# Performance work log

Hardware: AMD Instinct MI355X
Metric: run time of the kernel (lower is better)

Reference implementation:

```python
import jax, jax.numpy as jnp
import numpy as np

N_HEADS = 12
MAX_POS = 2048
SEQ = MAX_POS - 2  # seq_len_without_special = 2046
HEAD_DIM = 64
BATCH = 8


def setup_inputs() -> dict:
    key = jax.random.key(0)
    k1, k2, k3 = jax.random.split(key, 3)
    v = jax.random.normal(k1, (BATCH, MAX_POS, N_HEADS, HEAD_DIM), jnp.float32)
    offset = jax.random.normal(k2, (1, N_HEADS), jnp.float32)
    # learned bias base, torch init: uniform(-0.1, 0.1), shape [1, H, SEQ] (symmetric)
    w = jax.random.uniform(k3, (1, N_HEADS, SEQ), jnp.float32, -0.1, 0.1)
    return {"v": v, "offset": offset, "w": w}


def _fft_bias(v, offset, w):
    # strip special tokens ([CLS]/[SEP])
    v_ = v[:, 1:-1, :, :]                      # [B, S, H, D]
    B, S, H, D = v_.shape
    # --- symmetric circulant base z of length 2S-1 ---
    w_ = w[..., :S]                            # [1, H, S]
    z = jnp.concatenate(
        [w_[..., -1:], jnp.flip(w_[..., 1:], axis=-1), w_[..., :-1]], axis=-1
    )                                          # [1, H, 2S-1]
    z = z - offset[..., None]                  # broadcast offset per head
    z = jnp.exp(z)                             # feature_map == 'exp'
    z_fft = jnp.fft.rfft(z)                    # [1, H, S] complex (len 2S-1 odd -> m=S)

    pad = S - 1                                # symmetric: pad_size = seq_len - 1
    v_p = jnp.transpose(v_, (0, 3, 2, 1))      # [B, D, H, S]
    v_p = jnp.pad(v_p, ((0, 0), (0, 0), (0, 0), (pad, 0)))  # left-pad to 2S-1
    v_fft = jnp.fft.rfft(v_p)                  # [B, D, H, S]
    # torch.irfft(x, 1) with default signal_sizes infers even length 2*(m-1)=2S-2
    pbv = jnp.fft.irfft(v_fft * z_fft)[..., :S]  # [B, D, H, S]
    pbv = jnp.pad(pbv, ((0, 0), (0, 0), (0, 0), (1, 1)))     # restore special slots
    pbv = jnp.transpose(pbv, (0, 3, 2, 1))     # [B, S+2, H, D]

    o = jnp.pad(jnp.ones((S,), v.dtype), (pad, 0))           # [2S-1]
    o_fft = jnp.fft.rfft(o)                    # [S]
    z_pb = jnp.fft.irfft(z_fft * o_fft)[..., :S]             # [1, H, S]
    z_pb = jnp.pad(z_pb, ((0, 0), (0, 0), (1, 1)))           # [1, H, S+2]
    z_pb = jnp.swapaxes(z_pb, -2, -1)          # [1, S+2, H]
    return pbv, z_pb


def reference(v, offset, w):
    return _fft_bias(v, offset, w)
```

## Files before the change

### kernel.cpp

```cpp
#include <hip/hip_runtime.h>
#include <hip/hip_bf16.h>

#define BATCH 8
#define MAXPOS 2048
#define SEQ 2046
#define NH 12
#define HD 64
#define NCSLOT 254
#define TSTEPS 64
#define PLANE (NH * HD)

typedef __attribute__((ext_vector_type(4))) float floatx4;
typedef __attribute__((ext_vector_type(8))) short shortx8;

#define ATILE_BYTES (NH * NCSLOT * 512 * 2)

#define GLOAD_LDS16(src, dst)                                                  \
    __builtin_amdgcn_global_load_lds(                                          \
        (const __attribute__((address_space(1))) void*)(src),                  \
        (__attribute__((address_space(3))) void*)(dst), 16, 0, 0)

#define NB_V2  (BATCH * TSTEPS)
#define NB_ZPB NH
#define NB_A   (NCSLOT * NH)

__global__ __launch_bounds__(256)
void prep_all(const float* __restrict__ v, const float* __restrict__ w,
              const float* __restrict__ off, ushort* __restrict__ atile,
              ushort* __restrict__ vbf, float* __restrict__ out) {
    __shared__ __align__(16) char smem[32 * 768 * 2];
    const int bi  = blockIdx.x;
    const int tid = threadIdx.x;

    if (bi < NB_V2) {
        ushort (*L)[768] = (ushort(*)[768])smem;
        const int b  = bi >> 6;
        const int tc = bi & 63;
        const int t0 = tc * 32;
        const float* vb = v + (size_t)(b * MAXPOS + 1 + t0) * PLANE;
#pragma unroll
        for (int i = 0; i < 24; ++i) {
            const int f = i * 256 + tid;
            const int r = f / 192;
            const int s = f - r * 192;
            float4 val = make_float4(0.f, 0.f, 0.f, 0.f);
            if (t0 + r < SEQ) val = *(const float4*)(vb + (size_t)f * 4);
            __hip_bfloat16 c0 = __float2bfloat16(val.x);
            __hip_bfloat16 c1 = __float2bfloat16(val.y);
            __hip_bfloat16 c2 = __float2bfloat16(val.z);
            __hip_bfloat16 c3 = __float2bfloat16(val.w);
            ushort4 pk;
            pk.x = *(ushort*)&c0; pk.y = *(ushort*)&c1;
            pk.z = *(ushort*)&c2; pk.w = *(ushort*)&c3;
            *(ushort4*)&L[r][(s * 4) ^ ((r >> 3) * 16)] = pk;
        }
        __syncthreads();
        const int wv   = tid >> 6;
        const int lane = tid & 63;
        const int q    = lane >> 4;
        const int dcol = lane & 15;
        const int cb   = wv * 16 + dcol;
#pragma unroll
        for (int h = 0; h < NH; ++h) {
            const int pc = (h * 64 + cb) ^ (q * 16);
            ushort pk[8];
#pragma unroll
            for (int j = 0; j < 8; ++j) pk[j] = L[q * 8 + j][pc];
            *(uint4*)(vbf + ((size_t)((b * NH + h) * TSTEPS + tc) * 4 + wv) * 512 + lane * 8) = *(uint4*)pk;
        }
    } else if (bi < NB_V2 + NB_ZPB) {
        float* Es   = (float*)smem;
        float* Ss   = (float*)smem + 2048;
        float* wsum = (float*)smem + 4096;
        const int h    = bi - NB_V2;
        const int wid  = tid >> 6;
        const int lane = tid & 63;
        const float offh = off[h];
        const float* wh  = w + h * SEQ;
        for (int i = tid; i < SEQ; i += 256) Es[i] = __expf(wh[i] - offh);
        __syncthreads();
        const int base = tid * 8;
        float loc[8];
        float s = 0.f;
#pragma unroll
        for (int j = 0; j < 8; ++j) {
            float e = (base + j < SEQ) ? Es[base + j] : 0.f;
            s += e; loc[j] = s;
        }
        float sc = s;
#pragma unroll
        for (int d = 1; d < 64; d <<= 1) {
            float t = __shfl_up(sc, d);
            if (lane >= d) sc += t;
        }
        if (lane == 63) wsum[wid] = sc;
        __syncthreads();
        float woff = 0.f;
        for (int k = 0; k < wid; ++k) woff += wsum[k];
        float prefix = woff + sc - s;
#pragma unroll
        for (int j = 0; j < 8; ++j)
            if (base + j < SEQ) Ss[base + j] = prefix + loc[j];
        __syncthreads();
        const float E0 = Es[0];
        const size_t zb = (size_t)BATCH * MAXPOS * PLANE;
        for (int i = tid; i < SEQ; i += 256)
            out[zb + (size_t)(i + 1) * NH + h] = Ss[i] + Ss[SEQ - 1 - i] - E0;
    } else if (bi < NB_V2 + NB_ZPB + NB_A) {
        const int idx   = bi - NB_V2 - NB_ZPB;
        const int cslot = idx % NCSLOT;
        const int h     = idx / NCSLOT;
        const float offh = off[h];
        const float* wh  = w + h * SEQ;
        const int ci   = cslot - 127;
        const int lane = tid >> 2;
        const int jp   = (tid & 3) * 2;
        const int q    = lane >> 4;
        const int m    = lane & 15;
        const int d0   = 16 * ci + q * 8 - m + jp;
        ushort pk[2];
#pragma unroll
        for (int e = 0; e < 2; ++e) {
            int k = d0 + e; k = (k < 0) ? -k : k;
            float val = (k < SEQ) ? __expf(wh[k] - offh) : 0.f;
            __hip_bfloat16 bv = __float2bfloat16(val);
            pk[e] = *(ushort*)&bv;
        }
        *(ushort2*)(atile + ((size_t)(h * NCSLOT + cslot) * 512 + lane * 8 + jp)) = *(ushort2*)pk;
    } else {
        const int i = (bi - NB_V2 - NB_ZPB - NB_A) * 256 + tid;
        if (i < 2 * BATCH * PLANE) {
            int side = i / (BATCH * PLANE);
            int r    = i % (BATCH * PLANE);
            int b    = r / PLANE;
            int j    = r % PLANE;
            int p    = side ? (MAXPOS - 1) : 0;
            out[((size_t)b * MAXPOS + p) * PLANE + j] = 0.f;
        }
        if (i < 2 * NH) {
            size_t zb = (size_t)BATCH * MAXPOS * PLANE;
            int p = (i < NH) ? 0 : (MAXPOS - 1);
            out[zb + (size_t)p * NH + (i % NH)] = 0.f;
        }
    }
}


#define WBAR                                                                   \
  do {                                                                         \
    if (wvu < 2) asm volatile("s_waitcnt vmcnt(2)\n\ts_barrier" ::: "memory"); \
    else         asm volatile("s_waitcnt vmcnt(1)\n\ts_barrier" ::: "memory"); \
  } while (0)
#define WBAR0 asm volatile("s_waitcnt vmcnt(0)\n\ts_barrier" ::: "memory")

#define STEP(T4, E, STG)                                                       \
  do {                                                                         \
    const int abE = ab + 2 * (E);                                              \
    shortx8 bf[4];                                                             \
    a2 = a0; a3 = a1;                                                          \
    a0 = *(const shortx8*)(&As[(abE) & 31][lane8]);                            \
    a1 = *(const shortx8*)(&As[(abE - 1) & 31][lane8]);                        \
    _Pragma("unroll")                                                          \
    for (int dt = 0; dt < 4; ++dt)                                             \
        bf[dt] = *(const shortx8*)(&Bs[T4][dt][lane8]);                        \
    if (STG) {                                                                 \
        if (wvu < 2)                                                           \
            GLOAD_LDS16(aSt + (E) * 1024, &As[(csw + 2 * (E)) & 31][0]);       \
        GLOAD_LDS16(bSt + (E) * 2048, &Bs[((T4) + 2) & 3][wvu][0]);            \
    }                                                                          \
    __builtin_amdgcn_s_setprio(1);                                             \
    _Pragma("unroll")                                                          \
    for (int dt = 0; dt < 4; ++dt)                                             \
        acc[2][dt] = __builtin_amdgcn_mfma_f32_16x16x32_bf16(a2, bf[dt], acc[2][dt], 0, 0, 0); \
    _Pragma("unroll")                                                          \
    for (int dt = 0; dt < 4; ++dt)                                             \
        acc[3][dt] = __builtin_amdgcn_mfma_f32_16x16x32_bf16(a3, bf[dt], acc[3][dt], 0, 0, 0); \
    _Pragma("unroll")                                                          \
    for (int dt = 0; dt < 4; ++dt)                                             \
        acc[0][dt] = __builtin_amdgcn_mfma_f32_16x16x32_bf16(a0, bf[dt], acc[0][dt], 0, 0, 0); \
    _Pragma("unroll")                                                          \
    for (int dt = 0; dt < 4; ++dt)                                             \
        acc[1][dt] = __builtin_amdgcn_mfma_f32_16x16x32_bf16(a1, bf[dt], acc[1][dt], 0, 0, 0); \
    __builtin_amdgcn_s_setprio(0);                                             \
  } while (0)

__global__ __launch_bounds__(256, 3)
void gemm_pbv(const ushort* __restrict__ atile, const ushort* __restrict__ vbf,
              float* __restrict__ out) {
    __shared__ short As[32][512];
    __shared__ short Bs[4][4][512];

    const int bid  = blockIdx.x;
    const int l    = (bid & 7) * 96 + (bid >> 3);
    const int g    = l >> 3;
    const int nt   = l & 7;
    const int h    = g >> 3;
    const int bb   = g & 7;
    const int tid  = threadIdx.x;
    const int wvu  = __builtin_amdgcn_readfirstlane(tid >> 6);
    const int lane = tid & 63;
    const int lane8 = lane * 8;
    const int nt16  = nt * 16;

    floatx4 acc[4][4];
#pragma unroll
    for (int s = 0; s < 4; ++s)
#pragma unroll
        for (int dt = 0; dt < 4; ++dt) acc[s][dt] = (floatx4){0.f, 0.f, 0.f, 0.f};

    const ushort* aBase  = atile + (size_t)h * NCSLOT * 512;
    const ushort* bPanel = vbf + (size_t)(bb * NH + h) * (TSTEPS * 4 * 512);

    {
        const int cbase = 112 - nt16;
        const int j0 = (wvu == 0) ? 0 : (wvu == 1) ? 5 : (wvu == 2) ? 10 : 14;
        const int j1 = (wvu == 0) ? 5 : (wvu == 1) ? 10 : (wvu == 2) ? 14 : 18;
        for (int j = j0; j < j1; ++j) {
            const int cs = cbase + j;
            GLOAD_LDS16(aBase + (size_t)cs * 512 + lane8, &As[cs & 31][0]);
        }
        GLOAD_LDS16(bPanel + (0 * 4 + wvu) * 512 + lane8, &Bs[0][wvu][0]);
        GLOAD_LDS16(bPanel + (1 * 4 + wvu) * 512 + lane8, &Bs[1][wvu][0]);
    }
    WBAR0;

    int ab  = 127 - nt16 - 4 * wvu;
    int csw = 131 - nt16 - wvu;
    const ushort* aSt = aBase + (size_t)(131 - nt16 - wvu) * 512 + lane8;
    const ushort* bSt = bPanel + (2 * 4 + wvu) * 512 + lane8;

    shortx8 a0, a1, a2, a3;
    a0 = *(const shortx8*)(&As[(ab - 2) & 31][lane8]);
    a1 = *(const shortx8*)(&As[(ab - 3) & 31][lane8]);

    for (int u = 0; u < 15; ++u) {
        STEP(0, 0, 1); WBAR;
        STEP(1, 1, 1); WBAR;
        STEP(2, 2, 1); WBAR;
        STEP(3, 3, 1); WBAR;
        ab += 8; csw += 8; aSt += 4 * 1024; bSt += 4 * 2048;
    }
    STEP(0, 0, 1); WBAR;
    STEP(1, 1, 1); WBAR;
    STEP(2, 2, 0); WBAR0;
    STEP(3, 3, 0);

    const int q    = lane >> 4;
    const int dcol = lane & 15;
    const int nB   = nt * 256 + wvu * 64;
#pragma unroll
    for (int s = 0; s < 4; ++s) {
        int nsb = nB + s * 16 + q * 4;
#pragma unroll
        for (int r = 0; r < 4; ++r) {
            int n = nsb + r;
            if (n < SEQ) {
                float* ob = out + ((size_t)(bb * MAXPOS + 1 + n) * NH + h) * HD + dcol;
#pragma unroll
                for (int dt = 0; dt < 4; ++dt) ob[dt * 16] = acc[s][dt][r];
            }
        }
    }
}

extern "C" void kernel_launch(void* const* d_in, const int* in_sizes, int n_in,
                              void* d_out, int out_size, void* d_ws, size_t ws_size,
                              hipStream_t stream) {
    const float* v   = (const float*)d_in[0];
    const float* off = (const float*)d_in[1];
    const float* w   = (const float*)d_in[2];
    float* out = (float*)d_out;

    ushort* atile = (ushort*)d_ws;
    ushort* vbf   = (ushort*)((char*)d_ws + ATILE_BYTES);

    prep_all<<<NB_V2 + NB_ZPB + NB_A + 48, 256, 0, stream>>>(v, w, off, atile, vbf, out);
    gemm_pbv<<<768, 256, 0, stream>>>(atile, vbf, out);
}
```

Measured before the change: 135.7 us.

## Split prep kernel and software-pipeline GEMM fragment loads across barrier

The fused prep kernel becomes two kernels, one for the bf16 repack of v and one for the bias tile, zpb and zero-fill work, so each launch has uniform block types and smaller LDS use. The GEMM main loop now uses three-deep B staging and double-buffered A/B register fragments. The next step's LDS reads are issued between the two halves of the MFMA work, after the vmcnt wait, with a single barrier at the end of each step, so LDS latency hides behind MFMAs. This adds an extra kernel launch and more register pressure at three blocks per CU.

After: 142.1 us. 4.7% more time.

```diff
diff --git a/kernel.cpp b/kernel.cpp
--- a/kernel.cpp
+++ b/kernel.cpp
@@ -25,54 +25,57 @@
 #define NB_A   (NCSLOT * NH)
 
 __global__ __launch_bounds__(256)
-void prep_all(const float* __restrict__ v, const float* __restrict__ w,
-              const float* __restrict__ off, ushort* __restrict__ atile,
-              ushort* __restrict__ vbf, float* __restrict__ out) {
-    __shared__ __align__(16) char smem[32 * 768 * 2];
+void prep_v(const float* __restrict__ v, ushort* __restrict__ vbf) {
+    __shared__ __align__(16) ushort L[32][768];
     const int bi  = blockIdx.x;
     const int tid = threadIdx.x;
-
-    if (bi < NB_V2) {
-        ushort (*L)[768] = (ushort(*)[768])smem;
-        const int b  = bi >> 6;
-        const int tc = bi & 63;
-        const int t0 = tc * 32;
-        const float* vb = v + (size_t)(b * MAXPOS + 1 + t0) * PLANE;
-#pragma unroll
-        for (int i = 0; i < 24; ++i) {
-            const int f = i * 256 + tid;
-            const int r = f / 192;
-            const int s = f - r * 192;
-            float4 val = make_float4(0.f, 0.f, 0.f, 0.f);
-            if (t0 + r < SEQ) val = *(const float4*)(vb + (size_t)f * 4);
-            __hip_bfloat16 c0 = __float2bfloat16(val.x);
-            __hip_bfloat16 c1 = __float2bfloat16(val.y);
-            __hip_bfloat16 c2 = __float2bfloat16(val.z);
-            __hip_bfloat16 c3 = __float2bfloat16(val.w);
-            ushort4 pk;
-            pk.x = *(ushort*)&c0; pk.y = *(ushort*)&c1;
-            pk.z = *(ushort*)&c2; pk.w = *(ushort*)&c3;
-            *(ushort4*)&L[r][(s * 4) ^ ((r >> 3) * 16)] = pk;
-        }
-        __syncthreads();
-        const int wv   = tid >> 6;
-        const int lane = tid & 63;
-        const int q    = lane >> 4;
-        const int dcol = lane & 15;
-        const int cb   = wv * 16 + dcol;
-#pragma unroll
-        for (int h = 0; h < NH; ++h) {
-            const int pc = (h * 64 + cb) ^ (q * 16);
-            ushort pk[8];
-#pragma unroll
-            for (int j = 0; j < 8; ++j) pk[j] = L[q * 8 + j][pc];
-            *(uint4*)(vbf + ((size_t)((b * NH + h) * TSTEPS + tc) * 4 + wv) * 512 + lane * 8) = *(uint4*)pk;
-        }
-    } else if (bi < NB_V2 + NB_ZPB) {
-        float* Es   = (float*)smem;
-        float* Ss   = (float*)smem + 2048;
-        float* wsum = (float*)smem + 4096;
-        const int h    = bi - NB_V2;
+    const int b  = bi >> 6;
+    const int tc = bi & 63;
+    const int t0 = tc * 32;
+    const float* vb = v + (size_t)(b * MAXPOS + 1 + t0) * PLANE;
+#pragma unroll
+    for (int i = 0; i < 24; ++i) {
+        const int f = i * 256 + tid;
+        const int r = f / 192;
+        const int s = f - r * 192;
+        float4 val = make_float4(0.f, 0.f, 0.f, 0.f);
+        if (t0 + r < SEQ) val = *(const float4*)(vb + (size_t)f * 4);
+        __hip_bfloat16 c0 = __float2bfloat16(val.x);
+        __hip_bfloat16 c1 = __float2bfloat16(val.y);
+        __hip_bfloat16 c2 = __float2bfloat16(val.z);
+        __hip_bfloat16 c3 = __float2bfloat16(val.w);
+        ushort4 pk;
+        pk.x = *(ushort*)&c0; pk.y = *(ushort*)&c1;
+        pk.z = *(ushort*)&c2; pk.w = *(ushort*)&c3;
+        *(ushort4*)&L[r][(s * 4) ^ ((r >> 3) * 16)] = pk;
+    }
+    __syncthreads();
+    const int wv   = tid >> 6;
+    const int lane = tid & 63;
+    const int q    = lane >> 4;
+    const int dcol = lane & 15;
+    const int cb   = wv * 16 + dcol;
+#pragma unroll
+    for (int h = 0; h < NH; ++h) {
+        const int pc = (h * 64 + cb) ^ (q * 16);
+        ushort pk[8];
+#pragma unroll
+        for (int j = 0; j < 8; ++j) pk[j] = L[q * 8 + j][pc];
+        *(uint4*)(vbf + ((size_t)((b * NH + h) * TSTEPS + tc) * 4 + wv) * 512 + lane * 8) = *(uint4*)pk;
+    }
+}
+
+__global__ __launch_bounds__(256)
+void prep_rest(const float* __restrict__ w, const float* __restrict__ off,
+               ushort* __restrict__ atile, float* __restrict__ out) {
+    const int bi  = blockIdx.x;
+    const int tid = threadIdx.x;
+
+    if (bi < NB_ZPB) {
+        __shared__ float Es[SEQ];
+        __shared__ float Ss[SEQ];
+        __shared__ float wsum[4];
+        const int h    = bi;
         const int wid  = tid >> 6;
         const int lane = tid & 63;
         const float offh = off[h];
@@ -106,8 +109,8 @@
         const size_t zb = (size_t)BATCH * MAXPOS * PLANE;
         for (int i = tid; i < SEQ; i += 256)
             out[zb + (size_t)(i + 1) * NH + h] = Ss[i] + Ss[SEQ - 1 - i] - E0;
-    } else if (bi < NB_V2 + NB_ZPB + NB_A) {
-        const int idx   = bi - NB_V2 - NB_ZPB;
+    } else if (bi < NB_ZPB + NB_A) {
+        const int idx   = bi - NB_ZPB;
         const int cslot = idx % NCSLOT;
         const int h     = idx / NCSLOT;
         const float offh = off[h];
@@ -128,7 +131,7 @@
         }
         *(ushort2*)(atile + ((size_t)(h * NCSLOT + cslot) * 512 + lane * 8 + jp)) = *(ushort2*)pk;
     } else {
-        const int i = (bi - NB_V2 - NB_ZPB - NB_A) * 256 + tid;
+        const int i = (bi - NB_ZPB - NB_A) * 256 + tid;
         if (i < 2 * BATCH * PLANE) {
             int side = i / (BATCH * PLANE);
             int r    = i % (BATCH * PLANE);
@@ -146,42 +149,47 @@
 }
 
 
-#define WBAR                                                                   \
+#define WAITC                                                                  \
   do {                                                                         \
-    if (wvu < 2) asm volatile("s_waitcnt vmcnt(2)\n\ts_barrier" ::: "memory"); \
-    else         asm volatile("s_waitcnt vmcnt(1)\n\ts_barrier" ::: "memory"); \
+    if (wvu < 2) asm volatile("s_waitcnt vmcnt(2)" ::: "memory");              \
+    else         asm volatile("s_waitcnt vmcnt(1)" ::: "memory");              \
   } while (0)
-#define WBAR0 asm volatile("s_waitcnt vmcnt(0)\n\ts_barrier" ::: "memory")
-
-#define STEP(T4, E, STG)                                                       \
+#define WAIT0 asm volatile("s_waitcnt vmcnt(0)" ::: "memory")
+#define BARRIER asm volatile("s_barrier" ::: "memory")
+
+#define STEP(T4, E, AO0, AO1, AN0, AN1, BC, BN, STG, W0, ER)                   \
   do {                                                                         \
-    const int abE = ab + 2 * (E);                                              \
-    shortx8 bf[4];                                                             \
-    a2 = a0; a3 = a1;                                                          \
-    a0 = *(const shortx8*)(&As[(abE) & 31][lane8]);                            \
-    a1 = *(const shortx8*)(&As[(abE - 1) & 31][lane8]);                        \
-    _Pragma("unroll")                                                          \
-    for (int dt = 0; dt < 4; ++dt)                                             \
-        bf[dt] = *(const shortx8*)(&Bs[T4][dt][lane8]);                        \
     if (STG) {                                                                 \
         if (wvu < 2)                                                           \
             GLOAD_LDS16(aSt + (E) * 1024, &As[(csw + 2 * (E)) & 31][0]);       \
-        GLOAD_LDS16(bSt + (E) * 2048, &Bs[((T4) + 2) & 3][wvu][0]);            \
+        GLOAD_LDS16(bSt + (E) * 2048, &Bs[((T4) + 3) & 3][wvu][0]);            \
     }                                                                          \
     __builtin_amdgcn_s_setprio(1);                                             \
     _Pragma("unroll")                                                          \
     for (int dt = 0; dt < 4; ++dt)                                             \
-        acc[2][dt] = __builtin_amdgcn_mfma_f32_16x16x32_bf16(a2, bf[dt], acc[2][dt], 0, 0, 0); \
-    _Pragma("unroll")                                                          \
-    for (int dt = 0; dt < 4; ++dt)                                             \
-        acc[3][dt] = __builtin_amdgcn_mfma_f32_16x16x32_bf16(a3, bf[dt], acc[3][dt], 0, 0, 0); \
-    _Pragma("unroll")                                                          \
-    for (int dt = 0; dt < 4; ++dt)                                             \
-        acc[0][dt] = __builtin_amdgcn_mfma_f32_16x16x32_bf16(a0, bf[dt], acc[0][dt], 0, 0, 0); \
-    _Pragma("unroll")                                                          \
-    for (int dt = 0; dt < 4; ++dt)                                             \
-        acc[1][dt] = __builtin_amdgcn_mfma_f32_16x16x32_bf16(a1, bf[dt], acc[1][dt], 0, 0, 0); \
+        acc[2][dt] = __builtin_amdgcn_mfma_f32_16x16x32_bf16(AO0, BC[dt], acc[2][dt], 0, 0, 0); \
+    _Pragma("unroll")                                                          \
+    for (int dt = 0; dt < 4; ++dt)                                             \
+        acc[3][dt] = __builtin_amdgcn_mfma_f32_16x16x32_bf16(AO1, BC[dt], acc[3][dt], 0, 0, 0); \
     __builtin_amdgcn_s_setprio(0);                                             \
+    if (W0) { WAIT0; } else { WAITC; }                                         \
+    if (ER) {                                                                  \
+        AO0 = *(const shortx8*)(&As[(ab + 2 * (E) + 2) & 31][lane8]);          \
+        AO1 = *(const shortx8*)(&As[(ab + 2 * (E) + 1) & 31][lane8]);          \
+        _Pragma("unroll")                                                      \
+        for (int dt = 0; dt < 4; ++dt)                                         \
+            BN[dt] = *(const shortx8*)(&Bs[((T4) + 1) & 3][dt][lane8]);        \
+        __builtin_amdgcn_sched_barrier(0);                                     \
+    }                                                                          \
+    __builtin_amdgcn_s_setprio(1);                                             \
+    _Pragma("unroll")                                                          \
+    for (int dt = 0; dt < 4; ++dt)                                             \
+        acc[0][dt] = __builtin_amdgcn_mfma_f32_16x16x32_bf16(AN0, BC[dt], acc[0][dt], 0, 0, 0); \
+    _Pragma("unroll")                                                          \
+    for (int dt = 0; dt < 4; ++dt)                                             \
+        acc[1][dt] = __builtin_amdgcn_mfma_f32_16x16x32_bf16(AN1, BC[dt], acc[1][dt], 0, 0, 0); \
+    __builtin_amdgcn_s_setprio(0);                                             \
+    BARRIER;                                                                   \
   } while (0)
 
 __global__ __launch_bounds__(256, 3)
@@ -213,37 +221,40 @@
 
     {
         const int cbase = 112 - nt16;
-        const int j0 = (wvu == 0) ? 0 : (wvu == 1) ? 5 : (wvu == 2) ? 10 : 14;
-        const int j1 = (wvu == 0) ? 5 : (wvu == 1) ? 10 : (wvu == 2) ? 14 : 18;
-        for (int j = j0; j < j1; ++j) {
+        for (int j = wvu * 5; j < wvu * 5 + 5; ++j) {
             const int cs = cbase + j;
             GLOAD_LDS16(aBase + (size_t)cs * 512 + lane8, &As[cs & 31][0]);
         }
         GLOAD_LDS16(bPanel + (0 * 4 + wvu) * 512 + lane8, &Bs[0][wvu][0]);
         GLOAD_LDS16(bPanel + (1 * 4 + wvu) * 512 + lane8, &Bs[1][wvu][0]);
-    }
-    WBAR0;
+        GLOAD_LDS16(bPanel + (2 * 4 + wvu) * 512 + lane8, &Bs[2][wvu][0]);
+    }
+    WAIT0; BARRIER;
 
     int ab  = 127 - nt16 - 4 * wvu;
-    int csw = 131 - nt16 - wvu;
-    const ushort* aSt = aBase + (size_t)(131 - nt16 - wvu) * 512 + lane8;
-    const ushort* bSt = bPanel + (2 * 4 + wvu) * 512 + lane8;
-
-    shortx8 a0, a1, a2, a3;
-    a0 = *(const shortx8*)(&As[(ab - 2) & 31][lane8]);
-    a1 = *(const shortx8*)(&As[(ab - 3) & 31][lane8]);
+    int csw = 133 - nt16 - wvu;
+    const ushort* aSt = aBase + (size_t)(133 - nt16 - wvu) * 512 + lane8;
+    const ushort* bSt = bPanel + (3 * 4 + wvu) * 512 + lane8;
+
+    shortx8 ax0, ax1, ay0, ay1, bx[4], by[4];
+    ax0 = *(const shortx8*)(&As[(ab - 2) & 31][lane8]);
+    ax1 = *(const shortx8*)(&As[(ab - 3) & 31][lane8]);
+    ay0 = *(const shortx8*)(&As[(ab) & 31][lane8]);
+    ay1 = *(const shortx8*)(&As[(ab - 1) & 31][lane8]);
+#pragma unroll
+    for (int dt = 0; dt < 4; ++dt) bx[dt] = *(const shortx8*)(&Bs[0][dt][lane8]);
 
     for (int u = 0; u < 15; ++u) {
-        STEP(0, 0, 1); WBAR;
-        STEP(1, 1, 1); WBAR;
-        STEP(2, 2, 1); WBAR;
-        STEP(3, 3, 1); WBAR;
+        STEP(0, 0, ax0, ax1, ay0, ay1, bx, by, 1, 0, 1);
+        STEP(1, 1, ay0, ay1, ax0, ax1, by, bx, 1, 0, 1);
+        STEP(2, 2, ax0, ax1, ay0, ay1, bx, by, 1, 0, 1);
+        STEP(3, 3, ay0, ay1, ax0, ax1, by, bx, 1, 0, 1);
         ab += 8; csw += 8; aSt += 4 * 1024; bSt += 4 * 2048;
     }
-    STEP(0, 0, 1); WBAR;
-    STEP(1, 1, 1); WBAR;
-    STEP(2, 2, 0); WBAR0;
-    STEP(3, 3, 0);
+    STEP(0, 0, ax0, ax1, ay0, ay1, bx, by, 1, 0, 1);
+    STEP(1, 1, ay0, ay1, ax0, ax1, by, bx, 0, 1, 1);
+    STEP(2, 2, ax0, ax1, ay0, ay1, bx, by, 0, 1, 1);
+    STEP(3, 3, ay0, ay1, ax0, ax1, by, bx, 0, 1, 0);
 
     const int q    = lane >> 4;
     const int dcol = lane & 15;
@@ -274,6 +285,7 @@
     ushort* atile = (ushort*)d_ws;
     ushort* vbf   = (ushort*)((char*)d_ws + ATILE_BYTES);
 
-    prep_all<<<NB_V2 + NB_ZPB + NB_A + 48, 256, 0, stream>>>(v, w, off, atile, vbf, out);
+    prep_v<<<NB_V2, 256, 0, stream>>>(v, vbf);
+    prep_rest<<<NB_ZPB + NB_A + 48, 256, 0, stream>>>(w, off, atile, out);
     gemm_pbv<<<768, 256, 0, stream>>>(atile, vbf, out);
 }
```

## Retile GEMM warps to 2x2 grid with 8 row-slots by 2 column tiles

Applied to the files above, without the earlier changes.

Changes the per-wave tile of the Toeplitz GEMM from 64 rows by all 64 output columns to 128 rows by 32 columns, arranging the four waves as a 2x2 grid. Each step now reads two B fragments instead of four, while keeping eight shifted A fragments in a register rotation. The intent is to cut LDS traffic for B per MFMA and rebalance register use. In exchange, more A registers stay live, which may raise register pressure at launch bound 3, and the prologue A staging and initial fragment setup change.

Result: no change. 137.0 us (+1.0%).

```diff
diff --git a/kernel.cpp b/kernel.cpp
--- a/kernel.cpp
+++ b/kernel.cpp
@@ -153,34 +153,27 @@
   } while (0)
 #define WBAR0 asm volatile("s_waitcnt vmcnt(0)\n\ts_barrier" ::: "memory")
 
+#define MFMA_S(S, A)                                                           \
+    acc[S][0] = __builtin_amdgcn_mfma_f32_16x16x32_bf16(A, bf0, acc[S][0], 0, 0, 0); \
+    acc[S][1] = __builtin_amdgcn_mfma_f32_16x16x32_bf16(A, bf1, acc[S][1], 0, 0, 0);
+
 #define STEP(T4, E, STG)                                                       \
   do {                                                                         \
     const int abE = ab + 2 * (E);                                              \
-    shortx8 bf[4];                                                             \
-    a2 = a0; a3 = a1;                                                          \
+    shortx8 bf0, bf1;                                                          \
+    a7 = a5; a6 = a4; a5 = a3; a4 = a2; a3 = a1; a2 = a0;                      \
     a0 = *(const shortx8*)(&As[(abE) & 31][lane8]);                            \
     a1 = *(const shortx8*)(&As[(abE - 1) & 31][lane8]);                        \
-    _Pragma("unroll")                                                          \
-    for (int dt = 0; dt < 4; ++dt)                                             \
-        bf[dt] = *(const shortx8*)(&Bs[T4][dt][lane8]);                        \
+    bf0 = *(const shortx8*)(&Bs[T4][wd2][lane8]);                              \
+    bf1 = *(const shortx8*)(&Bs[T4][wd2 + 1][lane8]);                          \
     if (STG) {                                                                 \
         if (wvu < 2)                                                           \
             GLOAD_LDS16(aSt + (E) * 1024, &As[(csw + 2 * (E)) & 31][0]);       \
         GLOAD_LDS16(bSt + (E) * 2048, &Bs[((T4) + 2) & 3][wvu][0]);            \
     }                                                                          \
     __builtin_amdgcn_s_setprio(1);                                             \
-    _Pragma("unroll")                                                          \
-    for (int dt = 0; dt < 4; ++dt)                                             \
-        acc[2][dt] = __builtin_amdgcn_mfma_f32_16x16x32_bf16(a2, bf[dt], acc[2][dt], 0, 0, 0); \
-    _Pragma("unroll")                                                          \
-    for (int dt = 0; dt < 4; ++dt)                                             \
-        acc[3][dt] = __builtin_amdgcn_mfma_f32_16x16x32_bf16(a3, bf[dt], acc[3][dt], 0, 0, 0); \
-    _Pragma("unroll")                                                          \
-    for (int dt = 0; dt < 4; ++dt)                                             \
-        acc[0][dt] = __builtin_amdgcn_mfma_f32_16x16x32_bf16(a0, bf[dt], acc[0][dt], 0, 0, 0); \
-    _Pragma("unroll")                                                          \
-    for (int dt = 0; dt < 4; ++dt)                                             \
-        acc[1][dt] = __builtin_amdgcn_mfma_f32_16x16x32_bf16(a1, bf[dt], acc[1][dt], 0, 0, 0); \
+    MFMA_S(2, a2) MFMA_S(3, a3) MFMA_S(4, a4) MFMA_S(5, a5)                    \
+    MFMA_S(6, a6) MFMA_S(7, a7) MFMA_S(0, a0) MFMA_S(1, a1)                    \
     __builtin_amdgcn_s_setprio(0);                                             \
   } while (0)
 
@@ -201,21 +194,21 @@
     const int lane = tid & 63;
     const int lane8 = lane * 8;
     const int nt16  = nt * 16;
-
-    floatx4 acc[4][4];
-#pragma unroll
-    for (int s = 0; s < 4; ++s)
-#pragma unroll
-        for (int dt = 0; dt < 4; ++dt) acc[s][dt] = (floatx4){0.f, 0.f, 0.f, 0.f};
+    const int wn    = wvu >> 1;
+    const int wd2   = (wvu & 1) * 2;
+
+    floatx4 acc[8][2];
+#pragma unroll
+    for (int s = 0; s < 8; ++s)
+#pragma unroll
+        for (int dt = 0; dt < 2; ++dt) acc[s][dt] = (floatx4){0.f, 0.f, 0.f, 0.f};
 
     const ushort* aBase  = atile + (size_t)h * NCSLOT * 512;
     const ushort* bPanel = vbf + (size_t)(bb * NH + h) * (TSTEPS * 4 * 512);
 
     {
         const int cbase = 112 - nt16;
-        const int j0 = (wvu == 0) ? 0 : (wvu == 1) ? 5 : (wvu == 2) ? 10 : 14;
-        const int j1 = (wvu == 0) ? 5 : (wvu == 1) ? 10 : (wvu == 2) ? 14 : 18;
-        for (int j = j0; j < j1; ++j) {
+        for (int j = wvu * 5; j < wvu * 5 + 5; ++j) {
             const int cs = cbase + j;
             GLOAD_LDS16(aBase + (size_t)cs * 512 + lane8, &As[cs & 31][0]);
         }
@@ -224,14 +217,19 @@
     }
     WBAR0;
 
-    int ab  = 127 - nt16 - 4 * wvu;
+    int ab  = 127 - nt16 - 8 * wn;
     int csw = 131 - nt16 - wvu;
     const ushort* aSt = aBase + (size_t)(131 - nt16 - wvu) * 512 + lane8;
     const ushort* bSt = bPanel + (2 * 4 + wvu) * 512 + lane8;
 
-    shortx8 a0, a1, a2, a3;
+    shortx8 a0, a1, a2, a3, a4, a5, a6, a7;
     a0 = *(const shortx8*)(&As[(ab - 2) & 31][lane8]);
     a1 = *(const shortx8*)(&As[(ab - 3) & 31][lane8]);
+    a2 = *(const shortx8*)(&As[(ab - 4) & 31][lane8]);
+    a3 = *(const shortx8*)(&As[(ab - 5) & 31][lane8]);
+    a4 = *(const shortx8*)(&As[(ab - 6) & 31][lane8]);
+    a5 = *(const shortx8*)(&As[(ab - 7) & 31][lane8]);
+    a6 = a0; a7 = a0;
 
     for (int u = 0; u < 15; ++u) {
         STEP(0, 0, 1); WBAR;
@@ -247,17 +245,18 @@
 
     const int q    = lane >> 4;
     const int dcol = lane & 15;
-    const int nB   = nt * 256 + wvu * 64;
-#pragma unroll
-    for (int s = 0; s < 4; ++s) {
+    const int nB   = nt * 256 + wn * 128;
+    const int cB   = wd2 * 16 + dcol;
+#pragma unroll
+    for (int s = 0; s < 8; ++s) {
         int nsb = nB + s * 16 + q * 4;
 #pragma unroll
         for (int r = 0; r < 4; ++r) {
             int n = nsb + r;
             if (n < SEQ) {
-                float* ob = out + ((size_t)(bb * MAXPOS + 1 + n) * NH + h) * HD + dcol;
-#pragma unroll
-                for (int dt = 0; dt < 4; ++dt) ob[dt * 16] = acc[s][dt][r];
+                float* ob = out + ((size_t)(bb * MAXPOS + 1 + n) * NH + h) * HD + cB;
+#pragma unroll
+                for (int dt = 0; dt < 2; ++dt) ob[dt * 16] = acc[s][dt][r];
             }
         }
     }
```
